# Optimization experiments

Hardware: AMD Instinct MI355X
Metric: run time of the kernel (lower is better)

## Reference

```python
import jax, jax.numpy as jnp
import numpy as np

EMBED_DIM = 2048
NUM_HEADS = 16
BLOCK_SIZE = 128


def setup_inputs() -> dict:
    key = jax.random.key(0)
    k1, k2, k3 = jax.random.split(key, 3)
    B, S, E = 2, 4096, EMBED_DIM
    x = jax.random.normal(k1, (B, S, E), dtype=jnp.float32)
    # small init so attention logits are in a sane range
    w_qkv = jax.random.normal(k2, (3 * E, E), dtype=jnp.float32) * 0.02
    w_out = jax.random.normal(k3, (E, E), dtype=jnp.float32) * 0.02
    b_out = jnp.zeros((E,), dtype=jnp.float32)
    return {"x": x, "w_qkv": w_qkv, "w_out": w_out, "b_out": b_out}


def _flash_attention_v2(q, k, v, block_size, scale):
    # q,k,v: [B,H,S,D]; S divisible by block_size.
    # Faithful to the torch module, including its extra l_ij factor in the
    # output rescaling (out += beta*l_ij/l_new * (p @ v)).
    B, H, S, D = q.shape
    nb = S // block_size
    qb = q.reshape(B, H, nb, block_size, D)          # all query blocks at once
    kb = k.reshape(B, H, nb, block_size, D).transpose(2, 0, 1, 3, 4)  # [nb,B,H,bs,D]
    vb = v.reshape(B, H, nb, block_size, D).transpose(2, 0, 1, 3, 4)

    out0 = jnp.zeros_like(qb)
    l0 = jnp.zeros((B, H, nb, block_size, 1), dtype=q.dtype)
    m0 = jnp.full((B, H, nb, block_size, 1), -jnp.inf, dtype=q.dtype)

    def step(carry, kv):
        out, l, m = carry
        k_j, v_j = kv  # [B,H,bs,D]
        s = jnp.einsum('bhnqd,bhkd->bhnqk', qb, k_j) * scale  # [B,H,nb,bs,bs]
        m_ij = jnp.max(s, axis=-1, keepdims=True)
        p = jnp.exp(s - m_ij)
        l_ij = jnp.sum(p, axis=-1, keepdims=True)
        m_new = jnp.maximum(m, m_ij)
        alpha = jnp.exp(m - m_new)
        beta = jnp.exp(m_ij - m_new)
        l_new = alpha * l + beta * l_ij
        pv = jnp.einsum('bhnqk,bhkd->bhnqd', p, v_j)
        out_new = (alpha * l / l_new) * out + (beta * l_ij / l_new) * pv
        return (out_new, l_new, m_new), None

    (out, _, _), _ = jax.lax.scan(step, (out0, l0, m0), (kb, vb))
    return out.reshape(B, H, S, D)


def reference(x, w_qkv, w_out, b_out):
    B, S, E = x.shape
    H = NUM_HEADS
    D = E // H
    scale = 1.0 / np.sqrt(D).astype(np.float32)
    qkv = (x @ w_qkv.T).reshape(B, S, 3, H, D)
    q, k, v = jnp.moveaxis(qkv, 2, 0)            # each [B,S,H,D]
    q = q.transpose(0, 2, 1, 3)                   # [B,H,S,D]
    k = k.transpose(0, 2, 1, 3)
    v = v.transpose(0, 2, 1, 3)
    out = _flash_attention_v2(q, k, v, BLOCK_SIZE, scale)  # [B,H,S,D]
    out = out.transpose(0, 2, 1, 3).reshape(B, S, E)
    return out @ w_out.T + b_out
```

## Files before the change

kernel.cpp:

```cpp
#include <hip/hip_runtime.h>
#include <hip/hip_bf16.h>
#include <stdint.h>

#define DEV __device__ __forceinline__

typedef __attribute__((ext_vector_type(8))) short short8;
typedef __attribute__((ext_vector_type(4))) float f32x4;

#define B_ 2
#define S_ 4096
#define E_ 2048
#define H_ 16
#define D_ 128

#define BAR() asm volatile("s_barrier" ::: "memory")
#define LGKM0() asm volatile("s_waitcnt lgkmcnt(0)" ::: "memory")
#define VMC(N) asm volatile("s_waitcnt vmcnt(" #N ")" ::: "memory")

DEV unsigned short f2bf(float x) {
  union { float f; uint32_t u; } a; a.f = x;
  uint32_t r = a.u + 0x7fffu + ((a.u >> 16) & 1u);
  return (unsigned short)(r >> 16);
}

DEV unsigned int cvt_pk_bf16(float a, float b) {
  unsigned int r;
  asm("v_cvt_pk_bf16_f32 %0, %1, %2" : "=v"(r) : "v"(a), "v"(b));
  return r;
}

DEV float exp2f_(float x) { return __builtin_amdgcn_exp2f(x); }

DEV void glds16(const void* g, void* l) {
  __builtin_amdgcn_global_load_lds(
      (const __attribute__((address_space(1))) uint32_t*)g,
      (__attribute__((address_space(3))) uint32_t*)l, 16, 0, 0);
}

__global__ __launch_bounds__(256) void cvtk3(
    const float* __restrict__ x, const float* __restrict__ wq,
    const float* __restrict__ wo, unsigned short* __restrict__ xb,
    unsigned short* __restrict__ wqb, unsigned short* __restrict__ wob) {
  const int n1 = (B_ * S_ * E_) / 4, n2 = (3 * E_ * E_) / 4, n3 = (E_ * E_) / 4;
  int i = blockIdx.x * blockDim.x + threadIdx.x;
  int stride = gridDim.x * blockDim.x;
  for (; i < n1 + n2 + n3; i += stride) {
    const float4* s;
    ushort4* d;
    int j;
    if (i < n1) { s = (const float4*)x; d = (ushort4*)xb; j = i; }
    else if (i < n1 + n2) { s = (const float4*)wq; d = (ushort4*)wqb; j = i - n1; }
    else { s = (const float4*)wo; d = (ushort4*)wob; j = i - n1 - n2; }
    float4 v = s[j];
    ushort4 o;
    o.x = f2bf(v.x); o.y = f2bf(v.y); o.z = f2bf(v.z); o.w = f2bf(v.w);
    d[j] = o;
  }
}

template<int OUT_F32>
__global__ __launch_bounds__(512, 2) void gemm256(
    const unsigned short* __restrict__ A,
    const unsigned short* __restrict__ Bm,
    void* __restrict__ Cp,
    const float* __restrict__ bias,
    int M, int N, int K, int nbn)
{
  __shared__ __align__(16) unsigned char lds[131072];
  const int NT = K >> 6;
  const int K2 = K * 2;
  int cpx = gridDim.x >> 3;
  int bid = (blockIdx.x & 7) * cpx + (blockIdx.x >> 3);
  int bm = bid / nbn, bn = bid % nbn;
  int m0 = bm * 256, n0 = bn * 256;
  int t = threadIdx.x, lane = t & 63, wv = t >> 6;
  int lo = lane & 15, hi = lane >> 4;
  int wm = wv >> 2, wn = wv & 3;

  int colsw = ((t & 7) * 16) ^ (((t >> 3) & 7) << 4);
  const unsigned char* gA = (const unsigned char*)A + (size_t)(m0 + (t >> 3)) * K2 + colsw;
  const unsigned char* gB = (const unsigned char*)Bm + (size_t)(n0 + (t >> 3)) * K2 + colsw;

  int swzl = (lo & 7) << 4;
  int colk0 = (hi * 16) ^ swzl;
  int colk1 = (64 + hi * 16) ^ swzl;
  unsigned char* rdA = lds + wm * 16384 + lo * 128;
  unsigned char* rdB = lds + 32768 + (wn >> 1) * 16384 + ((wn & 1) * 64 + lo) * 128;

  f32x4 acc[8][4] = {};

  auto STG = [&](int isA, int d, int h, int kt) {
    if (kt >= NT) return;
    const unsigned char* g = (isA ? gA : gB) + (size_t)h * 128 * K2 + (size_t)kt * 128;
    unsigned char* l = lds + (isA ? 0 : 32768) + d * 65536 + h * 16384 + wv * 1024;
    glds16(g, l);
    glds16(g + (size_t)64 * K2, l + 8192);
  };
  auto DSA = [&](int d, int g4, int colk, short8* dst) {
#pragma unroll
    for (int i = 0; i < 4; ++i)
      dst[i] = *(const short8*)(rdA + d * 65536 + (g4 * 4 + i) * 2048 + colk);
  };
  auto DSB = [&](int d, int colk, short8* dst) {
#pragma unroll
    for (int i = 0; i < 4; ++i)
      dst[i] = *(const short8*)(rdB + d * 65536 + i * 2048 + colk);
  };
  auto MM = [&](int g4, short8* a, short8* b) {
    __builtin_amdgcn_s_setprio(1);
#pragma unroll
    for (int i = 0; i < 4; ++i)
#pragma unroll
      for (int j = 0; j < 4; ++j)
        acc[g4 * 4 + i][j] =
            __builtin_amdgcn_mfma_f32_16x16x32_bf16(a[i], b[j], acc[g4 * 4 + i][j], 0, 0, 0);
    __builtin_amdgcn_s_setprio(0);
  };

  STG(1, 0, 0, 0); STG(1, 0, 1, 0); STG(0, 0, 0, 0); STG(0, 0, 1, 0);
  STG(0, 1, 0, 1); STG(0, 1, 1, 1);
  VMC(4);
  BAR();

  short8 aT[4], aU[4], b0[4], b1[4];
  const int TL = (NT >> 1) - 1;
  for (int it = 0; it <= TL; ++it) {
    int j0 = 2 * it;
    DSA(0, 0, colk0, aT); DSB(0, colk0, b0);
    STG(1, 1, 0, j0 + 1);
    BAR(); MM(0, aT, b0); LGKM0(); BAR();
    DSA(0, 1, colk0, aU); DSB(0, colk1, b1);
    STG(1, 1, 1, j0 + 1);
    BAR(); MM(1, aU, b0); LGKM0(); BAR();
    DSA(0, 0, colk1, aT);
    STG(0, 0, 0, j0 + 2);
    BAR(); MM(0, aT, b1); LGKM0(); BAR();
    DSA(0, 1, colk1, aU);
    STG(0, 0, 1, j0 + 2);
    BAR(); MM(1, aU, b1); LGKM0();
    if (it == TL) { VMC(0); } else { VMC(4); }
    BAR();
    DSA(1, 0, colk0, aT); DSB(1, colk0, b0);
    STG(1, 0, 0, j0 + 2);
    BAR(); MM(0, aT, b0); LGKM0(); BAR();
    DSA(1, 1, colk0, aU); DSB(1, colk1, b1);
    STG(1, 0, 1, j0 + 2);
    BAR(); MM(1, aU, b0); LGKM0(); BAR();
    DSA(1, 0, colk1, aT);
    STG(0, 1, 0, j0 + 3);
    BAR(); MM(0, aT, b1); LGKM0(); BAR();
    DSA(1, 1, colk1, aU);
    STG(0, 1, 1, j0 + 3);
    BAR(); MM(1, aU, b1); LGKM0(); VMC(4);
    BAR();
  }

  if constexpr (OUT_F32) {
    float* C = (float*)Cp;
#pragma unroll
    for (int mf = 0; mf < 8; ++mf)
#pragma unroll
      for (int nf = 0; nf < 4; ++nf) {
        int row = m0 + wm * 128 + mf * 16 + hi * 4;
        int col = n0 + wn * 64 + nf * 16 + lo;
        float bv = bias[col];
#pragma unroll
        for (int r = 0; r < 4; ++r)
          C[(size_t)(row + r) * N + col] = acc[mf][nf][r] + bv;
      }
  } else {
    unsigned short* C = (unsigned short*)Cp;
#pragma unroll
    for (int mf = 0; mf < 8; ++mf)
#pragma unroll
      for (int nf = 0; nf < 4; ++nf) {
        int row = m0 + wm * 128 + mf * 16 + hi * 4;
        int col = n0 + wn * 64 + nf * 16 + lo;
#pragma unroll
        for (int r = 0; r < 4; ++r)
          C[(size_t)(row + r) * N + col] = f2bf(acc[mf][nf][r]);
      }
  }
}

__global__ __launch_bounds__(256) void transpose_v(const unsigned short* __restrict__ qkv,
                                                   unsigned short* __restrict__ vt) {
  __shared__ __align__(16) unsigned char tl[32768];
  int bid = blockIdx.x;
  int st = bid & 31, bh = bid >> 5;
  int h = bh & 15, b = bh >> 4;
  int s0 = st * 128;
  int t = threadIdx.x, c = t & 15, rr = t >> 4;
#pragma unroll
  for (int i = 0; i < 8; ++i) {
    int s = rr + i * 16;
    const unsigned short* g = qkv + ((((size_t)b * S_ + s0 + s) * 3 + 2) * H_ + h) * D_ + c * 8;
    *(uint4*)(tl + s * 256 + ((c * 16) ^ (((s >> 3) & 7) << 4))) = *(const uint4*)g;
  }
  __syncthreads();
#pragma unroll
  for (int i = 0; i < 8; ++i) {
    int d = rr + i * 16;
    unsigned int w[4];
#pragma unroll
    for (int jj = 0; jj < 4; ++jj) {
      int s_a = c * 8 + jj * 2;
      unsigned int u0 = *(const unsigned short*)(tl + s_a * 256 + ((d * 2) ^ ((c & 7) << 4)));
      unsigned int u1 = *(const unsigned short*)(tl + (s_a + 1) * 256 + ((d * 2) ^ ((c & 7) << 4)));
      w[jj] = u0 | (u1 << 16);
    }
    uint4 val; val.x = w[0]; val.y = w[1]; val.z = w[2]; val.w = w[3];
    unsigned short* g = vt + (((size_t)b * H_ + h) * D_ + d) * S_ + s0 + c * 8;
    *(uint4*)g = val;
  }
}

__global__ __launch_bounds__(512, 2) void attn_fwd(
    const unsigned short* __restrict__ qkv,
    const unsigned short* __restrict__ vt,
    unsigned short* __restrict__ abuf)
{
  __shared__ __align__(16) unsigned char lds[65536];
  unsigned char* lK = lds;
  unsigned char* lV = lds + 32768;

  int bid = (blockIdx.x & 7) * 64 + (blockIdx.x >> 3);
  int qb = bid & 15, bh = bid >> 4;
  int h = bh & 15, b = bh >> 4;
  int t = threadIdx.x, lane = t & 63, wv = t >> 6;
  int hi = lane >> 4, lo = lane & 15;
  int q0 = qb * 256;
  const float c1 = 0.12751744f;

  short8 qf[2][4];
#pragma unroll
  for (int qj = 0; qj < 2; ++qj) {
    const unsigned short* qbase =
        qkv + ((((size_t)b * S_ + q0 + wv * 32 + qj * 16 + lo) * 3 + 0) * H_ + h) * D_;
#pragma unroll
    for (int ks = 0; ks < 4; ++ks)
      qf[qj][ks] = *(const short8*)(qbase + ks * 32 + hi * 8);
  }

  int sw = ((t & 15) * 16) ^ (((t >> 4) & 7) << 4);
  const unsigned char* gkb =
      (const unsigned char*)(qkv + (((size_t)b * S_ * 3 + 1) * H_ + h) * D_) +
      (size_t)(t >> 4) * 12288 + sw;
  const unsigned char* gvb =
      (const unsigned char*)(vt + ((size_t)b * H_ + h) * D_ * S_) +
      (size_t)(t >> 4) * 8192 + sw;
  unsigned char* lkd = lK + wv * 1024;
  unsigned char* lvd = lV + wv * 1024;

  f32x4 oacc[8][2] = {};
  float m_run[2] = {-__builtin_inff(), -__builtin_inff()};
  float l_run[2] = {0.f, 0.f};
  union PW { unsigned int u[4]; short8 s; };
  PW pp[2][4];

#pragma unroll
  for (int i = 0; i < 4; ++i) {
    glds16(gkb + i * 393216, lkd + i * 8192);
    glds16(gvb + i * 262144, lvd + i * 8192);
  }

  for (int jb = 0; jb < 32; ++jb) {
    VMC(0);
    BAR();

    f32x4 sacc[8][2];
    __builtin_amdgcn_s_setprio(1);
#pragma unroll
    for (int kf = 0; kf < 8; ++kf) {
      int kvr = kf * 16 + lo;
      int swz = (kvr & 7) << 4;
      sacc[kf][0] = f32x4{0.f, 0.f, 0.f, 0.f};
      sacc[kf][1] = f32x4{0.f, 0.f, 0.f, 0.f};
#pragma unroll
      for (int ks = 0; ks < 4; ++ks) {
        short8 kfr = *(const short8*)(lK + kvr * 256 + ((ks * 64 + hi * 16) ^ swz));
        sacc[kf][0] = __builtin_amdgcn_mfma_f32_16x16x32_bf16(kfr, qf[0][ks], sacc[kf][0], 0, 0, 0);
        sacc[kf][1] = __builtin_amdgcn_mfma_f32_16x16x32_bf16(kfr, qf[1][ks], sacc[kf][1], 0, 0, 0);
      }
    }
    __builtin_amdgcn_s_setprio(0);

    float m2[2], li[2], coef[2];
#pragma unroll
    for (int qj = 0; qj < 2; ++qj) {
      float mloc = -__builtin_inff();
#pragma unroll
      for (int kf = 0; kf < 8; ++kf)
#pragma unroll
        for (int r = 0; r < 4; ++r) mloc = fmaxf(mloc, sacc[kf][qj][r]);
      mloc = fmaxf(mloc, __shfl_xor(mloc, 16));
      mloc = fmaxf(mloc, __shfl_xor(mloc, 32));
      m2[qj] = mloc * c1;
      float lloc = 0.f;
#pragma unroll
      for (int kf = 0; kf < 8; ++kf)
#pragma unroll
        for (int r = 0; r < 4; ++r) {
          float p = exp2f_(fmaf(sacc[kf][qj][r], c1, -m2[qj]));
          sacc[kf][qj][r] = p;
          lloc += p;
        }
      lloc += __shfl_xor(lloc, 16);
      lloc += __shfl_xor(lloc, 32);
      li[qj] = lloc;
    }

    if (__all(m2[0] <= m_run[0] && m2[1] <= m_run[1])) {
#pragma unroll
      for (int qj = 0; qj < 2; ++qj) {
        coef[qj] = exp2f_(m2[qj] - m_run[qj]) * li[qj];
        l_run[qj] += coef[qj];
      }
    } else {
      float alpha[2];
#pragma unroll
      for (int qj = 0; qj < 2; ++qj) {
        float mn = fmaxf(m_run[qj], m2[qj]);
        alpha[qj] = exp2f_(m_run[qj] - mn);
        coef[qj] = exp2f_(m2[qj] - mn) * li[qj];
        l_run[qj] = alpha[qj] * l_run[qj] + coef[qj];
        m_run[qj] = mn;
      }
#pragma unroll
      for (int df = 0; df < 8; ++df)
#pragma unroll
        for (int qj = 0; qj < 2; ++qj)
#pragma unroll
          for (int r = 0; r < 4; ++r) oacc[df][qj][r] *= alpha[qj];
    }

#pragma unroll
    for (int qj = 0; qj < 2; ++qj) {
      float cf = coef[qj];
#pragma unroll
      for (int ks = 0; ks < 4; ++ks) {
        unsigned int a0 = cvt_pk_bf16(sacc[2 * ks][qj][0] * cf, sacc[2 * ks][qj][1] * cf);
        unsigned int b0 = cvt_pk_bf16(sacc[2 * ks + 1][qj][0] * cf, sacc[2 * ks + 1][qj][1] * cf);
        unsigned int a1 = cvt_pk_bf16(sacc[2 * ks][qj][2] * cf, sacc[2 * ks][qj][3] * cf);
        unsigned int b1 = cvt_pk_bf16(sacc[2 * ks + 1][qj][2] * cf, sacc[2 * ks + 1][qj][3] * cf);
        asm("v_permlane32_swap_b32 %0, %1" : "+v"(a0), "+v"(b0));
        asm("v_permlane16_swap_b32 %0, %1" : "+v"(a0), "+v"(b0));
        asm("v_permlane32_swap_b32 %0, %1" : "+v"(a1), "+v"(b1));
        asm("v_permlane16_swap_b32 %0, %1" : "+v"(a1), "+v"(b1));
        pp[qj][ks].u[0] = a0;
        pp[qj][ks].u[1] = a1;
        pp[qj][ks].u[2] = b0;
        pp[qj][ks].u[3] = b1;
      }
    }

    __builtin_amdgcn_s_setprio(1);
#pragma unroll
    for (int ks = 0; ks < 4; ++ks) {
#pragma unroll
      for (int df = 0; df < 8; ++df) {
        int dr = df * 16 + lo;
        short8 vf = *(const short8*)(lV + dr * 256 + ((ks * 64 + hi * 16) ^ ((dr & 7) << 4)));
        oacc[df][0] = __builtin_amdgcn_mfma_f32_16x16x32_bf16(vf, pp[0][ks].s, oacc[df][0], 0, 0, 0);
        oacc[df][1] = __builtin_amdgcn_mfma_f32_16x16x32_bf16(vf, pp[1][ks].s, oacc[df][1], 0, 0, 0);
      }
    }
    __builtin_amdgcn_s_setprio(0);

    BAR();
    if (jb < 31) {
      size_t kvK = (size_t)(jb + 1) * 1572864;
      size_t kvV = (size_t)(jb + 1) * 256;
#pragma unroll
      for (int i = 0; i < 4; ++i) {
        glds16(gkb + kvK + i * 393216, lkd + i * 8192);
        glds16(gvb + kvV + i * 262144, lvd + i * 8192);
      }
    }
  }

  BAR();
#pragma unroll
  for (int qj = 0; qj < 2; ++qj) {
    int rq = wv * 32 + qj * 16 + lo;
    int swzq = (rq & 7) << 4;
    float inv = 1.0f / l_run[qj];
#pragma unroll
    for (int df = 0; df < 8; ++df) {
      uint2 pk;
      pk.x = cvt_pk_bf16(oacc[df][qj][0] * inv, oacc[df][qj][1] * inv);
      pk.y = cvt_pk_bf16(oacc[df][qj][2] * inv, oacc[df][qj][3] * inv);
      *(uint2*)(lds + rq * 256 + ((df * 32 + hi * 8) ^ swzq)) = pk;
    }
  }
  __syncthreads();
#pragma unroll
  for (int i = 0; i < 8; ++i) {
    int row = i * 32 + (t >> 4);
    int c = t & 15;
    uint4 val = *(const uint4*)(lds + row * 256 + ((c * 16) ^ ((row & 7) << 4)));
    unsigned short* dst = abuf + (((size_t)b * S_ + q0 + row) * H_ + h) * D_ + c * 8;
    *(uint4*)dst = val;
  }
}

extern "C" void kernel_launch(void* const* d_in, const int* in_sizes, int n_in,
                              void* d_out, int out_size, void* d_ws, size_t ws_size,
                              hipStream_t stream) {
  const float* x = (const float*)d_in[0];
  const float* w_qkv = (const float*)d_in[1];
  const float* w_out = (const float*)d_in[2];
  const float* b_out = (const float*)d_in[3];
  float* out = (float*)d_out;
  char* ws = (char*)d_ws;

  unsigned short* xb    = (unsigned short*)(ws);
  unsigned short* wqkvb = (unsigned short*)(ws + 33554432);
  unsigned short* woutb = (unsigned short*)(ws + 58720256);
  unsigned short* qkvb  = (unsigned short*)(ws + 67108864);
  unsigned short* vtb   = (unsigned short*)(ws + 167772160);
  unsigned short* abuf  = xb;

  cvtk3<<<2048, 256, 0, stream>>>(x, w_qkv, w_out, xb, wqkvb, woutb);

  gemm256<0><<<768, 512, 0, stream>>>(xb, wqkvb, (void*)qkvb, nullptr,
                                      B_ * S_, 3 * E_, E_, 24);
  transpose_v<<<1024, 256, 0, stream>>>(qkvb, vtb);
  attn_fwd<<<512, 512, 0, stream>>>(qkvb, vtb, abuf);
  gemm256<1><<<256, 512, 0, stream>>>(abuf, woutb, (void*)out, b_out,
                                      B_ * S_, E_, E_, 8);
}
```

Measured before the change: 635.2 us.

## Fuse V transpose into QKV GEMM epilogue and drop transpose kernel

QKV GEMM tiles covering the V columns now stage their bf16 results through shared memory transposed and write directly into the head-major V^T buffer, then return. The separate transpose_v kernel is removed. This eliminates a launch and the extra global read and write of the V slice. It adds an LDS round-trip and a barrier to the epilogue of those tiles, and V is no longer written to the qkv buffer.

New measurement: 626.2 us. Within noise of the previous version (-1.4%).

```diff
diff --git a/kernel.cpp b/kernel.cpp
--- a/kernel.cpp
+++ b/kernel.cpp
@@ -58,12 +58,13 @@
   }
 }
 
-template<int OUT_F32>
+template<int OUT_F32, int VSPLIT>
 __global__ __launch_bounds__(512, 2) void gemm256(
     const unsigned short* __restrict__ A,
     const unsigned short* __restrict__ Bm,
     void* __restrict__ Cp,
     const float* __restrict__ bias,
+    unsigned short* __restrict__ vt,
     int M, int N, int K, int nbn)
 {
   __shared__ __align__(16) unsigned char lds[131072];
@@ -155,6 +156,36 @@
     BAR();
   }
 
+  if constexpr (VSPLIT) {
+    if (bn >= 16) {
+#pragma unroll
+      for (int mf = 0; mf < 8; ++mf)
+#pragma unroll
+        for (int nf = 0; nf < 4; ++nf) {
+          int row0 = wm * 128 + mf * 16 + hi * 4;
+          int col = wn * 64 + nf * 16 + lo;
+          uint2 pk;
+          pk.x = (unsigned int)f2bf(acc[mf][nf][0]) | ((unsigned int)f2bf(acc[mf][nf][1]) << 16);
+          pk.y = (unsigned int)f2bf(acc[mf][nf][2]) | ((unsigned int)f2bf(acc[mf][nf][3]) << 16);
+          *(uint2*)(lds + col * 512 + ((row0 * 2) ^ ((col & 7) << 4))) = pk;
+        }
+      __syncthreads();
+      int col = t & 255;
+      int half = t >> 8;
+      int nv = n0 + col - 4096;
+      int hh = nv >> 7, dd = nv & 127;
+      int b = m0 >> 12, s0 = m0 & 4095;
+      unsigned short* vrow = vt + (((size_t)b * H_ + hh) * D_ + dd) * S_ + s0;
+#pragma unroll
+      for (int jj = 0; jj < 16; ++jj) {
+        int j = half * 16 + jj;
+        uint4 v = *(const uint4*)(lds + col * 512 + 16 * (j ^ (col & 7)));
+        *(uint4*)(vrow + j * 8) = v;
+      }
+      return;
+    }
+  }
+
   if constexpr (OUT_F32) {
     float* C = (float*)Cp;
 #pragma unroll
@@ -180,38 +211,6 @@
         for (int r = 0; r < 4; ++r)
           C[(size_t)(row + r) * N + col] = f2bf(acc[mf][nf][r]);
       }
-  }
-}
-
-__global__ __launch_bounds__(256) void transpose_v(const unsigned short* __restrict__ qkv,
-                                                   unsigned short* __restrict__ vt) {
-  __shared__ __align__(16) unsigned char tl[32768];
-  int bid = blockIdx.x;
-  int st = bid & 31, bh = bid >> 5;
-  int h = bh & 15, b = bh >> 4;
-  int s0 = st * 128;
-  int t = threadIdx.x, c = t & 15, rr = t >> 4;
-#pragma unroll
-  for (int i = 0; i < 8; ++i) {
-    int s = rr + i * 16;
-    const unsigned short* g = qkv + ((((size_t)b * S_ + s0 + s) * 3 + 2) * H_ + h) * D_ + c * 8;
-    *(uint4*)(tl + s * 256 + ((c * 16) ^ (((s >> 3) & 7) << 4))) = *(const uint4*)g;
-  }
-  __syncthreads();
-#pragma unroll
-  for (int i = 0; i < 8; ++i) {
-    int d = rr + i * 16;
-    unsigned int w[4];
-#pragma unroll
-    for (int jj = 0; jj < 4; ++jj) {
-      int s_a = c * 8 + jj * 2;
-      unsigned int u0 = *(const unsigned short*)(tl + s_a * 256 + ((d * 2) ^ ((c & 7) << 4)));
-      unsigned int u1 = *(const unsigned short*)(tl + (s_a + 1) * 256 + ((d * 2) ^ ((c & 7) << 4)));
-      w[jj] = u0 | (u1 << 16);
-    }
-    uint4 val; val.x = w[0]; val.y = w[1]; val.z = w[2]; val.w = w[3];
-    unsigned short* g = vt + (((size_t)b * H_ + h) * D_ + d) * S_ + s0 + c * 8;
-    *(uint4*)g = val;
   }
 }
 
@@ -423,10 +422,9 @@
 
   cvtk3<<<2048, 256, 0, stream>>>(x, w_qkv, w_out, xb, wqkvb, woutb);
 
-  gemm256<0><<<768, 512, 0, stream>>>(xb, wqkvb, (void*)qkvb, nullptr,
-                                      B_ * S_, 3 * E_, E_, 24);
-  transpose_v<<<1024, 256, 0, stream>>>(qkvb, vtb);
+  gemm256<0, 1><<<768, 512, 0, stream>>>(xb, wqkvb, (void*)qkvb, nullptr, vtb,
+                                         B_ * S_, 3 * E_, E_, 24);
   attn_fwd<<<512, 512, 0, stream>>>(qkvb, vtb, abuf);
-  gemm256<1><<<256, 512, 0, stream>>>(abuf, woutb, (void*)out, b_out,
-                                      B_ * S_, E_, E_, 8);
-}
+  gemm256<1, 0><<<256, 512, 0, stream>>>(abuf, woutb, (void*)out, b_out, nullptr,
+                                         B_ * S_, E_, E_, 8);
+}
```
